# Kernel tuning notes

Hardware: AMD Instinct MI355X
Metric: run time of the kernel (lower is better)

Reference implementation:

```python
import jax, jax.numpy as jnp
import numpy as np

K = 11
EPS = 1e-6


def _box_sum(a):
    # a: [B, H, W] -> KxK zero-padded local sum (equivalent to nn.Unfold padding=K//2 then sum)
    return jax.lax.reduce_window(a, 0.0, jax.lax.add,
                                 window_dimensions=(1, K, K),
                                 window_strides=(1, 1, 1),
                                 padding='SAME')


def setup_inputs() -> dict:
    key = jax.random.key(0)
    k1, k2 = jax.random.split(key)
    x = jax.random.normal(k1, (8, 3, 1024, 1024), dtype=jnp.float32)
    y = jax.random.normal(k2, (8, 3, 1024, 1024), dtype=jnp.float32)
    return {"x": x, "y": y}


def reference(x, y):
    # Channel-reduce first, then local KxK box sums (math-identical to the
    # unfold-based sum over (C, K, K) with zero padding).
    xx = _box_sum((x * x).sum(axis=1))   # [B, H, W]
    yy = _box_sum((y * y).sum(axis=1))
    xy = _box_sum((x * y).sum(axis=1))
    x_norm = jnp.sqrt(xx)
    y_norm = jnp.sqrt(yy)
    return xy / (x_norm * y_norm + EPS)
```

## Files before the change

### kernel.cpp

```cpp
#include <hip/hip_runtime.h>
#include <math.h>

#define NB 8
#define NC 3
#define NH 1024
#define NW 1024
#define EPS 1e-6f

#define BAND 128
#define CH 32
#define KSTEPS (CH + 10)
#define PADW (BAND + 16)
#define NWAVES 4
#define NTHREADS 256

__global__ __launch_bounds__(NTHREADS)
void lcs_kernel(const float* __restrict__ x, const float* __restrict__ y,
                float* __restrict__ out) {
    __shared__ __align__(16) float P[NWAVES][3][PADW];

    const int tid = threadIdx.x;
    const int w   = tid >> 6;
    const int l   = tid & 63;

    const int gwid  = blockIdx.x * NWAVES + w;
    const int b     = gwid >> 8;
    const int rem   = gwid & 255;
    const int band0 = (rem & 7) * BAND;
    const int r0    = (rem >> 3) * CH;

    const size_t chan = (size_t)NH * NW;
    const float* xb = x + (size_t)b * NC * chan;
    const float* yb = y + (size_t)b * NC * chan;

    const int gc0 = band0 - 8 + 2 * l;
    const int gcE = band0 - 8 + 2 * (64 + l);
    const bool m0 = (gc0 >= 0);
    const bool mE = (l < 8) && (gcE < NW);

    float2 nx[3], ny[3], exv[3], eyv[3];

    auto ldrow = [&](int gr) {
        if ((unsigned)gr < (unsigned)NH) {
            const size_t ro = (size_t)gr * NW;
            #pragma unroll
            for (int c = 0; c < 3; ++c) {
                const float* xr = xb + c * chan + ro;
                const float* yr = yb + c * chan + ro;
                nx[c]  = m0 ? *(const float2*)(xr + gc0) : make_float2(0.f, 0.f);
                ny[c]  = m0 ? *(const float2*)(yr + gc0) : make_float2(0.f, 0.f);
                exv[c] = mE ? *(const float2*)(xr + gcE) : make_float2(0.f, 0.f);
                eyv[c] = mE ? *(const float2*)(yr + gcE) : make_float2(0.f, 0.f);
            }
        } else {
            #pragma unroll
            for (int c = 0; c < 3; ++c) {
                nx[c]  = make_float2(0.f, 0.f); ny[c]  = make_float2(0.f, 0.f);
                exv[c] = make_float2(0.f, 0.f); eyv[c] = make_float2(0.f, 0.f);
            }
        }
    };

    ldrow(r0 - 5);

    float2 ring[3][11];
    #pragma unroll
    for (int p = 0; p < 3; ++p)
        #pragma unroll
        for (int s = 0; s < 11; ++s) ring[p][s] = make_float2(0.f, 0.f);
    float2 vs[3] = {make_float2(0.f,0.f), make_float2(0.f,0.f), make_float2(0.f,0.f)};

    for (int g = 0; g < 4; ++g) {
        #pragma unroll
        for (int s = 0; s < 11; ++s) {
            const int k = g * 11 + s;
            if (k >= KSTEPS) continue;

            float2 pxx = make_float2(0.f,0.f), pyy = pxx, pxy = pxx;
            float2 qxx = pxx, qyy = pxx, qxy = pxx;
            #pragma unroll
            for (int c = 0; c < 3; ++c) {
                pxx.x += nx[c].x * nx[c].x;  pxx.y += nx[c].y * nx[c].y;
                pyy.x += ny[c].x * ny[c].x;  pyy.y += ny[c].y * ny[c].y;
                pxy.x += nx[c].x * ny[c].x;  pxy.y += nx[c].y * ny[c].y;
                qxx.x += exv[c].x * exv[c].x; qxx.y += exv[c].y * exv[c].y;
                qyy.x += eyv[c].x * eyv[c].x; qyy.y += eyv[c].y * eyv[c].y;
                qxy.x += exv[c].x * eyv[c].x; qxy.y += exv[c].y * eyv[c].y;
            }
            ((float2*)&P[w][0][0])[l] = pxx;
            ((float2*)&P[w][1][0])[l] = pyy;
            ((float2*)&P[w][2][0])[l] = pxy;
            if (l < 8) {
                ((float2*)&P[w][0][0])[64 + l] = qxx;
                ((float2*)&P[w][1][0])[64 + l] = qyy;
                ((float2*)&P[w][2][0])[64 + l] = qxy;
            }

            if (k + 1 < KSTEPS) ldrow(r0 - 4 + k);

            __builtin_amdgcn_wave_barrier();

            #pragma unroll
            for (int p = 0; p < 3; ++p) {
                const float* Pp = &P[w][p][0];
                float2 t[7];
                #pragma unroll
                for (int j = 0; j < 7; ++j)
                    t[j] = *(const float2*)(Pp + 2 * l + 2 + 2 * j);
                float h0 = ((t[0].y + t[1].x) + (t[1].y + t[2].x))
                         + ((t[2].y + t[3].x) + (t[3].y + t[4].x))
                         + ((t[4].y + t[5].x) + t[5].y);
                float h1 = h0 - t[0].y + t[6].x;
                vs[p].x += h0 - ring[p][s].x;
                vs[p].y += h1 - ring[p][s].y;
                ring[p][s].x = h0;
                ring[p][s].y = h1;
            }

            __builtin_amdgcn_wave_barrier();

            if (k >= 10) {
                const int orow = r0 + k - 10;
                float2 o;
                o.x = vs[2].x / (sqrtf(vs[0].x) * sqrtf(vs[1].x) + EPS);
                o.y = vs[2].y / (sqrtf(vs[0].y) * sqrtf(vs[1].y) + EPS);
                *(float2*)(out + ((size_t)b * NH + orow) * NW + band0 + 2 * l) = o;
            }
        }
    }
}

extern "C" void kernel_launch(void* const* d_in, const int* in_sizes, int n_in,
                              void* d_out, int out_size, void* d_ws, size_t ws_size,
                              hipStream_t stream) {
    const float* x = (const float*)d_in[0];
    const float* y = (const float*)d_in[1];
    float* out = (float*)d_out;
    lcs_kernel<<<dim3(512), dim3(NTHREADS), 0, stream>>>(x, y, out);
}
```

Baseline: 244.2 us.

## Use single-wave blocks, prefetch next row early, branchless masked loads, fast rcp/sqrt

Each block now holds a single 64-lane wave (2048 blocks) instead of four waves sharing a block. The next input row is loaded into a separate register buffer at the start of each step, so global-load latency overlaps the current row's compute. Boundary handling switches from predicated loads to clamped addresses plus multiplicative float masks, and the output uses hardware sqrt and reciprocal in place of division. The cost is higher register pressure from the doubled row buffers and slightly lower precision from the approximate reciprocal.

Measured after the change: 241.3 us. No clear change (-1.2%).

```diff
diff --git a/kernel.cpp b/kernel.cpp
--- a/kernel.cpp
+++ b/kernel.cpp
@@ -10,22 +10,17 @@
 #define BAND 128
 #define CH 32
 #define KSTEPS (CH + 10)
-#define PADW (BAND + 16)
-#define NWAVES 4
-#define NTHREADS 256
+#define PADW 144
 
-__global__ __launch_bounds__(NTHREADS)
+__global__ __launch_bounds__(64, 2)
 void lcs_kernel(const float* __restrict__ x, const float* __restrict__ y,
                 float* __restrict__ out) {
-    __shared__ __align__(16) float P[NWAVES][3][PADW];
+    __shared__ __align__(16) float P[3][PADW];
 
-    const int tid = threadIdx.x;
-    const int w   = tid >> 6;
-    const int l   = tid & 63;
-
-    const int gwid  = blockIdx.x * NWAVES + w;
-    const int b     = gwid >> 8;
-    const int rem   = gwid & 255;
+    const int l   = threadIdx.x;
+    const int bid = blockIdx.x;
+    const int b     = bid >> 8;
+    const int rem   = bid & 255;
     const int band0 = (rem & 7) * BAND;
     const int r0    = (rem >> 3) * CH;
 
@@ -34,34 +29,28 @@
     const float* yb = y + (size_t)b * NC * chan;
 
     const int gc0 = band0 - 8 + 2 * l;
-    const int gcE = band0 - 8 + 2 * (64 + l);
-    const bool m0 = (gc0 >= 0);
-    const bool mE = (l < 8) && (gcE < NW);
+    const int gcE = band0 + 120 + 2 * l;
+    const float mm = (gc0 >= 0) ? 1.f : 0.f;
+    const float me = (l < 8 && gcE + 1 <= NW - 1) ? 1.f : 0.f;
+    const int o0 = (gc0 >= 0) ? gc0 : 0;
+    const int oE = (me > 0.f) ? gcE : 0;
 
-    float2 nx[3], ny[3], exv[3], eyv[3];
-
-    auto ldrow = [&](int gr) {
-        if ((unsigned)gr < (unsigned)NH) {
-            const size_t ro = (size_t)gr * NW;
-            #pragma unroll
-            for (int c = 0; c < 3; ++c) {
-                const float* xr = xb + c * chan + ro;
-                const float* yr = yb + c * chan + ro;
-                nx[c]  = m0 ? *(const float2*)(xr + gc0) : make_float2(0.f, 0.f);
-                ny[c]  = m0 ? *(const float2*)(yr + gc0) : make_float2(0.f, 0.f);
-                exv[c] = mE ? *(const float2*)(xr + gcE) : make_float2(0.f, 0.f);
-                eyv[c] = mE ? *(const float2*)(yr + gcE) : make_float2(0.f, 0.f);
-            }
-        } else {
-            #pragma unroll
-            for (int c = 0; c < 3; ++c) {
-                nx[c]  = make_float2(0.f, 0.f); ny[c]  = make_float2(0.f, 0.f);
-                exv[c] = make_float2(0.f, 0.f); eyv[c] = make_float2(0.f, 0.f);
-            }
+    float2 cur[12], nxt[12];
+    auto ldrow = [&](int gr, float2* d) {
+        const int rc = gr < 0 ? 0 : (gr > NH - 1 ? NH - 1 : gr);
+        const size_t ro = (size_t)rc * NW;
+        #pragma unroll
+        for (int c = 0; c < 3; ++c) {
+            const float* xr = xb + c * chan + ro;
+            const float* yr = yb + c * chan + ro;
+            d[c]     = *(const float2*)(xr + o0);
+            d[3 + c] = *(const float2*)(yr + o0);
+            d[6 + c] = *(const float2*)(xr + oE);
+            d[9 + c] = *(const float2*)(yr + oE);
         }
     };
 
-    ldrow(r0 - 5);
+    ldrow(r0 - 5, cur);
 
     float2 ring[3][11];
     #pragma unroll
@@ -76,37 +65,46 @@
             const int k = g * 11 + s;
             if (k >= KSTEPS) continue;
 
+            if (k + 1 < KSTEPS) ldrow(r0 - 4 + k, nxt);
+
             float2 pxx = make_float2(0.f,0.f), pyy = pxx, pxy = pxx;
             float2 qxx = pxx, qyy = pxx, qxy = pxx;
             #pragma unroll
             for (int c = 0; c < 3; ++c) {
-                pxx.x += nx[c].x * nx[c].x;  pxx.y += nx[c].y * nx[c].y;
-                pyy.x += ny[c].x * ny[c].x;  pyy.y += ny[c].y * ny[c].y;
-                pxy.x += nx[c].x * ny[c].x;  pxy.y += nx[c].y * ny[c].y;
-                qxx.x += exv[c].x * exv[c].x; qxx.y += exv[c].y * exv[c].y;
-                qyy.x += eyv[c].x * eyv[c].x; qyy.y += eyv[c].y * eyv[c].y;
-                qxy.x += exv[c].x * eyv[c].x; qxy.y += exv[c].y * eyv[c].y;
+                const float2 xm = cur[c],   ym = cur[3+c];
+                const float2 xe = cur[6+c], ye = cur[9+c];
+                pxx.x += xm.x*xm.x; pxx.y += xm.y*xm.y;
+                pyy.x += ym.x*ym.x; pyy.y += ym.y*ym.y;
+                pxy.x += xm.x*ym.x; pxy.y += xm.y*ym.y;
+                qxx.x += xe.x*xe.x; qxx.y += xe.y*xe.y;
+                qyy.x += ye.x*ye.x; qyy.y += ye.y*ye.y;
+                qxy.x += xe.x*ye.x; qxy.y += xe.y*ye.y;
             }
-            ((float2*)&P[w][0][0])[l] = pxx;
-            ((float2*)&P[w][1][0])[l] = pyy;
-            ((float2*)&P[w][2][0])[l] = pxy;
+            const int gr = r0 - 5 + k;
+            const float rmf = (gr >= 0 && gr < NH) ? 1.f : 0.f;
+            const float cmM = rmf * mm, cmE = rmf * me;
+            pxx.x *= cmM; pxx.y *= cmM; pyy.x *= cmM; pyy.y *= cmM;
+            pxy.x *= cmM; pxy.y *= cmM;
+            qxx.x *= cmE; qxx.y *= cmE; qyy.x *= cmE; qyy.y *= cmE;
+            qxy.x *= cmE; qxy.y *= cmE;
+
+            ((float2*)&P[0][0])[l] = pxx;
+            ((float2*)&P[1][0])[l] = pyy;
+            ((float2*)&P[2][0])[l] = pxy;
             if (l < 8) {
-                ((float2*)&P[w][0][0])[64 + l] = qxx;
-                ((float2*)&P[w][1][0])[64 + l] = qyy;
-                ((float2*)&P[w][2][0])[64 + l] = qxy;
+                ((float2*)&P[0][0])[64 + l] = qxx;
+                ((float2*)&P[1][0])[64 + l] = qyy;
+                ((float2*)&P[2][0])[64 + l] = qxy;
             }
-
-            if (k + 1 < KSTEPS) ldrow(r0 - 4 + k);
-
             __builtin_amdgcn_wave_barrier();
 
             #pragma unroll
             for (int p = 0; p < 3; ++p) {
-                const float* Pp = &P[w][p][0];
+                const float* Pp = &P[p][0];
                 float2 t[7];
                 #pragma unroll
                 for (int j = 0; j < 7; ++j)
-                    t[j] = *(const float2*)(Pp + 2 * l + 2 + 2 * j);
+                    t[j] = *(const float2*)(Pp + 2*l + 2 + 2*j);
                 float h0 = ((t[0].y + t[1].x) + (t[1].y + t[2].x))
                          + ((t[2].y + t[3].x) + (t[3].y + t[4].x))
                          + ((t[4].y + t[5].x) + t[5].y);
@@ -116,15 +114,23 @@
                 ring[p][s].x = h0;
                 ring[p][s].y = h1;
             }
-
             __builtin_amdgcn_wave_barrier();
 
             if (k >= 10) {
                 const int orow = r0 + k - 10;
+                const float d0 = __builtin_amdgcn_sqrtf(vs[0].x) *
+                                 __builtin_amdgcn_sqrtf(vs[1].x) + EPS;
+                const float d1 = __builtin_amdgcn_sqrtf(vs[0].y) *
+                                 __builtin_amdgcn_sqrtf(vs[1].y) + EPS;
                 float2 o;
-                o.x = vs[2].x / (sqrtf(vs[0].x) * sqrtf(vs[1].x) + EPS);
-                o.y = vs[2].y / (sqrtf(vs[0].y) * sqrtf(vs[1].y) + EPS);
-                *(float2*)(out + ((size_t)b * NH + orow) * NW + band0 + 2 * l) = o;
+                o.x = vs[2].x * __builtin_amdgcn_rcpf(d0);
+                o.y = vs[2].y * __builtin_amdgcn_rcpf(d1);
+                *(float2*)(out + ((size_t)b * NH + orow) * NW + band0 + 2*l) = o;
+            }
+
+            if (k + 1 < KSTEPS) {
+                #pragma unroll
+                for (int i = 0; i < 12; ++i) cur[i] = nxt[i];
             }
         }
     }
@@ -136,5 +142,5 @@
     const float* x = (const float*)d_in[0];
     const float* y = (const float*)d_in[1];
     float* out = (float*)d_out;
-    lcs_kernel<<<dim3(512), dim3(NTHREADS), 0, stream>>>(x, y, out);
+    lcs_kernel<<<dim3(2048), dim3(64), 0, stream>>>(x, y, out);
 }
```
